# Optimization experiments

Hardware: AMD Instinct MI355X
Metric: run time of the kernel (lower is better)

The kernel has to match this reference:

```python
import jax, jax.numpy as jnp
import numpy as np

B, K, D = 16384, 2048, 128
T = 1.0

def setup_inputs() -> dict:
    key = jax.random.key(0)
    k1, k2 = jax.random.split(key)
    x = jax.random.normal(k1, (B, D), dtype=jnp.float32)
    # nn.init.normal_(center, std=0.01)
    center = jax.random.normal(k2, (K, D), dtype=jnp.float32) * 0.01
    return {"x": x, "center": center}

def _forward(x, center, temp):
    # Euclidean distance x[B,D] vs center[K,D] via expansion (avoids BxKxD blowup)
    x2 = jnp.sum(x * x, axis=-1, keepdims=True)          # [B,1]
    c2 = jnp.sum(center * center, axis=-1)               # [K]
    d2 = jnp.maximum(x2 + c2[None, :] - 2.0 * (x @ center.T), 0.0)  # [B,K]
    att_logit = -jnp.sqrt(d2) / temp                     # [B,K]
    # original detaches logits before softargmax
    logits = jax.lax.stop_gradient(att_logit)
    y_soft = jax.nn.softmax(logits / temp, axis=-1)      # [B,K]
    label = jnp.argmax(y_soft, axis=-1, keepdims=True)   # [B,1]
    y_hard = jax.nn.one_hot(label[:, 0], K, dtype=y_soft.dtype)  # [B,K]
    # straight-through estimator
    result = y_hard - jax.lax.stop_gradient(y_soft) + y_soft
    out = result @ center                                # [B,D]
    return out, center, label

def reference(x, center):
    return _forward(x, center, T)
```

## Files before the change

kernel.cpp:

```cpp
#include <hip/hip_runtime.h>
#include <cstdint>

#define NB 16384
#define NK 2048
#define ND 128
#define MARGIN 0.10f
#define CAP 2048
#define XPITCH 132

typedef __attribute__((ext_vector_type(8))) short bf16x8;
typedef __attribute__((ext_vector_type(4))) float f32x4;
typedef unsigned long long u64;

__device__ __forceinline__ unsigned short f2bf(float f) {
    unsigned u = __float_as_uint(f);
    u += 0x7fffu + ((u >> 16) & 1u);
    return (unsigned short)(u >> 16);
}

__global__ __launch_bounds__(256)
void prep(const float* __restrict__ c,
          unsigned short* __restrict__ cbf,
          float* __restrict__ c2,
          float* __restrict__ out_center) {
    const int bid = blockIdx.x;
    const int tid = threadIdx.x;
    if (bid < 128) {
        int t = bid * 256 + tid;
        int lane = t & 63, s = (t >> 6) & 3, kt = t >> 8;
        int kc = kt * 16 + (lane & 15);
        int d0 = s * 32 + (lane >> 4) * 8;
        const float* src = c + (long)kc * ND + d0;
        unsigned short h[8];
#pragma unroll
        for (int j = 0; j < 8; ++j) h[j] = f2bf(src[j]);
        int4 pk;
        pk.x = h[0] | (h[1] << 16); pk.y = h[2] | (h[3] << 16);
        pk.z = h[4] | (h[5] << 16); pk.w = h[6] | (h[7] << 16);
        ((int4*)cbf)[t] = pk;
    } else if (bid < 136) {
        int k = (bid - 128) * 256 + tid;
        const float4* row = (const float4*)(c + (long)k * ND);
        float s = 0.f;
#pragma unroll 8
        for (int i = 0; i < ND / 4; ++i) {
            float4 v = row[i];
            s += v.x * v.x + v.y * v.y + v.z * v.z + v.w * v.w;
        }
        c2[k] = s;
    } else {
        int i = (bid - 136) * 256 + tid;
        ((float4*)out_center)[i] = ((const float4*)c)[i];
    }
}

__global__ __launch_bounds__(512, 4)
void kmeans_main(const float* __restrict__ x,
                 const float* __restrict__ center,
                 const unsigned short* __restrict__ cbf,
                 const float* __restrict__ c2,
                 float* __restrict__ out,
                 float* __restrict__ label_out) {
    __shared__ float xs[32 * XPITCH];
    __shared__ float x2s[32];
    __shared__ unsigned bmin[32];
    __shared__ u64 best[32];
    __shared__ unsigned buf[CAP];
    __shared__ unsigned cnt;

    const int tid  = threadIdx.x;
    const int lane = tid & 63;
    const int wave = __builtin_amdgcn_readfirstlane(tid >> 6);
    const long rb  = (long)blockIdx.x * 32;

    {
        int idx = tid;
        int r = idx >> 5, q = idx & 31;
        ((float4*)(xs + r * XPITCH))[q] = ((const float4*)(x + (rb + r) * ND))[q];
        idx = tid + 512;
        r = idx >> 5; q = idx & 31;
        ((float4*)(xs + r * XPITCH))[q] = ((const float4*)(x + (rb + r) * ND))[q];
    }
    if (tid < 32) { bmin[tid] = 0x7f800000u; best[tid] = ~0ULL; }
    if (tid == 0) cnt = 0;
    __syncthreads();

    for (int i = 0; i < 4; ++i) {
        int r = wave * 4 + i;
        float2 v = *(const float2*)(xs + r * XPITCH + lane * 2);
        float s = v.x * v.x + v.y * v.y;
#pragma unroll
        for (int off = 32; off; off >>= 1) s += __shfl_xor(s, off, 64);
        if (lane == 0) x2s[r] = s;
    }
    __syncthreads();

    bf16x8 af[2][4];
#pragma unroll
    for (int rt = 0; rt < 2; ++rt)
#pragma unroll
        for (int s = 0; s < 4; ++s) {
            const float* p = xs + (rt * 16 + (lane & 15)) * XPITCH
                               + s * 32 + (lane >> 4) * 8;
            float4 u0 = ((const float4*)p)[0];
            float4 u1 = ((const float4*)p)[1];
            bf16x8 a;
            a[0] = (short)f2bf(u0.x); a[1] = (short)f2bf(u0.y);
            a[2] = (short)f2bf(u0.z); a[3] = (short)f2bf(u0.w);
            a[4] = (short)f2bf(u1.x); a[5] = (short)f2bf(u1.y);
            a[6] = (short)f2bf(u1.z); a[7] = (short)f2bf(u1.w);
            af[rt][s] = a;
        }

    float x2p[2][4];
#pragma unroll
    for (int rt = 0; rt < 2; ++rt)
#pragma unroll
        for (int reg = 0; reg < 4; ++reg)
            x2p[rt][reg] = x2s[rt * 16 + (lane >> 4) * 4 + reg];

    const bf16x8* CF = (const bf16x8*)cbf;
    const int kbase = wave * 256;

    float rmin[2][4];
#pragma unroll
    for (int rt = 0; rt < 2; ++rt)
#pragma unroll
        for (int reg = 0; reg < 4; ++reg) rmin[rt][reg] = __builtin_inff();

#pragma unroll 2
    for (int ct = 0; ct < 16; ++ct) {
        const int kt = (kbase >> 4) + ct;
        bf16x8 bf[4];
#pragma unroll
        for (int s = 0; s < 4; ++s) bf[s] = CF[(kt * 4 + s) * 64 + lane];
        f32x4 acc0 = {0.f,0.f,0.f,0.f}, acc1 = {0.f,0.f,0.f,0.f};
#pragma unroll
        for (int s = 0; s < 4; ++s) {
            acc0 = __builtin_amdgcn_mfma_f32_16x16x32_bf16(af[0][s], bf[s], acc0, 0,0,0);
            acc1 = __builtin_amdgcn_mfma_f32_16x16x32_bf16(af[1][s], bf[s], acc1, 0,0,0);
        }
        float c2v = c2[kt * 16 + (lane & 15)];
#pragma unroll
        for (int reg = 0; reg < 4; ++reg) {
            rmin[0][reg] = fminf(rmin[0][reg], fmaf(-2.f, acc0[reg], x2p[0][reg] + c2v));
            rmin[1][reg] = fminf(rmin[1][reg], fmaf(-2.f, acc1[reg], x2p[1][reg] + c2v));
        }
    }

#pragma unroll
    for (int rt = 0; rt < 2; ++rt)
#pragma unroll
        for (int reg = 0; reg < 4; ++reg) {
            float v = rmin[rt][reg];
#pragma unroll
            for (int off = 1; off < 16; off <<= 1)
                v = fminf(v, __shfl_xor(v, off, 64));
            if ((lane & 15) == 0)
                atomicMin(&bmin[rt * 16 + (lane >> 4) * 4 + reg], __float_as_uint(v));
        }
    __syncthreads();

    float thr[2][4];
#pragma unroll
    for (int rt = 0; rt < 2; ++rt)
#pragma unroll
        for (int reg = 0; reg < 4; ++reg)
            thr[rt][reg] = __uint_as_float(bmin[rt * 16 + (lane >> 4) * 4 + reg]) + MARGIN;

#pragma unroll 2
    for (int ct = 0; ct < 16; ++ct) {
        const int kt = (kbase >> 4) + ct;
        bf16x8 bf[4];
#pragma unroll
        for (int s = 0; s < 4; ++s) bf[s] = CF[(kt * 4 + s) * 64 + lane];
        f32x4 acc0 = {0.f,0.f,0.f,0.f}, acc1 = {0.f,0.f,0.f,0.f};
#pragma unroll
        for (int s = 0; s < 4; ++s) {
            acc0 = __builtin_amdgcn_mfma_f32_16x16x32_bf16(af[0][s], bf[s], acc0, 0,0,0);
            acc1 = __builtin_amdgcn_mfma_f32_16x16x32_bf16(af[1][s], bf[s], acc1, 0,0,0);
        }
        float c2v = c2[kt * 16 + (lane & 15)];
        const int col = kt * 16 + (lane & 15);
#pragma unroll
        for (int reg = 0; reg < 4; ++reg) {
            float d20 = fmaf(-2.f, acc0[reg], x2p[0][reg] + c2v);
            if (d20 <= thr[0][reg]) {
                unsigned rloc = (lane >> 4) * 4 + reg;
                unsigned idx = atomicAdd(&cnt, 1u);
                if (idx < CAP) buf[idx] = (rloc << 11) | (unsigned)col;
            }
            float d21 = fmaf(-2.f, acc1[reg], x2p[1][reg] + c2v);
            if (d21 <= thr[1][reg]) {
                unsigned rloc = 16 + (lane >> 4) * 4 + reg;
                unsigned idx = atomicAdd(&cnt, 1u);
                if (idx < CAP) buf[idx] = (rloc << 11) | (unsigned)col;
            }
        }
    }
    __syncthreads();

    unsigned n = cnt; if (n > CAP) n = CAP;
    for (unsigned i = tid; i < n; i += 512) {
        unsigned pc = buf[i];
        int rloc = pc >> 11, col = pc & (NK - 1);
        const float* xr = xs + rloc * XPITCH;
        const float* cr = center + (long)col * ND;
        float dot = 0.f;
#pragma unroll 8
        for (int d = 0; d < ND; ++d) dot = fmaf(xr[d], cr[d], dot);
        float t = x2s[rloc] + c2[col];
        float f = fmaxf(fmaf(-2.0f, dot, t), 0.0f);
        float s = __builtin_sqrtf(f);
        u64 key = ((u64)__float_as_uint(s) << 32) | (unsigned)col;
        atomicMin(&best[rloc], key);
    }
    __syncthreads();

    for (int i = 0; i < 4; ++i) {
        int rloc = wave * 4 + i;
        int bk = (int)(best[rloc] & 0xffffffffULL);
        float2 cv = ((const float2*)(center + (long)bk * ND))[lane];
        ((float2*)(out + (rb + rloc) * ND))[lane] = cv;
        if (lane == 0) label_out[rb + rloc] = (float)bk;
    }
}

extern "C" void kernel_launch(void* const* d_in, const int* in_sizes, int n_in,
                              void* d_out, int out_size, void* d_ws, size_t ws_size,
                              hipStream_t stream) {
    const float* x      = (const float*)d_in[0];
    const float* center = (const float*)d_in[1];
    float* out = (float*)d_out;

    float* out_x      = out;
    float* out_center = out + (long)NB * ND;
    float* out_label  = out_center + (long)NK * ND;

    unsigned short* cbf = (unsigned short*)d_ws;
    float* c2 = (float*)(cbf + (size_t)NK * ND);

    prep<<<392, 256, 0, stream>>>(center, cbf, c2, out_center);
    kmeans_main<<<NB / 32, 512, 0, stream>>>(x, center, cbf, c2,
                                             out_x, out_label);
}
```

Before: 97.67 us.

## Double rows per block to 64 and cache center norms in LDS

Each block now handles 64 query rows instead of 32. Every wave runs four 16-row MFMA tiles against each center fragment it loads, so each bf16 center load from global/L2 is reused twice as much. The center squared norms are staged once into shared memory rather than read from global inside the loops. In exchange, register and LDS use per block grow, occupancy drops to 2 blocks per CU, the grid halves to 256 blocks, and the candidate buffer of 2048 now serves twice as many rows, so it is more likely to overflow.

```diff
diff --git a/kernel.cpp b/kernel.cpp
--- a/kernel.cpp
+++ b/kernel.cpp
@@ -54,39 +54,38 @@
     }
 }
 
-__global__ __launch_bounds__(512, 4)
+__global__ __launch_bounds__(512, 2)
 void kmeans_main(const float* __restrict__ x,
                  const float* __restrict__ center,
                  const unsigned short* __restrict__ cbf,
                  const float* __restrict__ c2,
                  float* __restrict__ out,
                  float* __restrict__ label_out) {
-    __shared__ float xs[32 * XPITCH];
-    __shared__ float x2s[32];
-    __shared__ unsigned bmin[32];
-    __shared__ u64 best[32];
+    __shared__ float xs[64 * XPITCH];
+    __shared__ float c2s[NK];
+    __shared__ float x2s[64];
+    __shared__ unsigned bmin[64];
+    __shared__ u64 best[64];
     __shared__ unsigned buf[CAP];
     __shared__ unsigned cnt;
 
     const int tid  = threadIdx.x;
     const int lane = tid & 63;
     const int wave = __builtin_amdgcn_readfirstlane(tid >> 6);
-    const long rb  = (long)blockIdx.x * 32;
-
-    {
-        int idx = tid;
-        int r = idx >> 5, q = idx & 31;
+    const long rb  = (long)blockIdx.x * 64;
+
+#pragma unroll
+    for (int t = tid; t < 64 * 32; t += 512) {
+        int r = t >> 5, q = t & 31;
         ((float4*)(xs + r * XPITCH))[q] = ((const float4*)(x + (rb + r) * ND))[q];
-        idx = tid + 512;
-        r = idx >> 5; q = idx & 31;
-        ((float4*)(xs + r * XPITCH))[q] = ((const float4*)(x + (rb + r) * ND))[q];
-    }
-    if (tid < 32) { bmin[tid] = 0x7f800000u; best[tid] = ~0ULL; }
+    }
+    ((float4*)c2s)[tid] = ((const float4*)c2)[tid];
+    if (tid < 64) { bmin[tid] = 0x7f800000u; best[tid] = ~0ULL; }
     if (tid == 0) cnt = 0;
     __syncthreads();
 
-    for (int i = 0; i < 4; ++i) {
-        int r = wave * 4 + i;
+    for (int i = 0; i < 8; ++i) {
+        int r = wave * 8 + i;
         float2 v = *(const float2*)(xs + r * XPITCH + lane * 2);
         float s = v.x * v.x + v.y * v.y;
 #pragma unroll
@@ -95,9 +94,9 @@
     }
     __syncthreads();
 
-    bf16x8 af[2][4];
-#pragma unroll
-    for (int rt = 0; rt < 2; ++rt)
+    bf16x8 af[4][4];
+#pragma unroll
+    for (int rt = 0; rt < 4; ++rt)
 #pragma unroll
         for (int s = 0; s < 4; ++s) {
             const float* p = xs + (rt * 16 + (lane & 15)) * XPITCH
@@ -112,44 +111,47 @@
             af[rt][s] = a;
         }
 
-    float x2p[2][4];
-#pragma unroll
-    for (int rt = 0; rt < 2; ++rt)
+    float x2p[4][4];
+#pragma unroll
+    for (int rt = 0; rt < 4; ++rt)
 #pragma unroll
         for (int reg = 0; reg < 4; ++reg)
             x2p[rt][reg] = x2s[rt * 16 + (lane >> 4) * 4 + reg];
 
     const bf16x8* CF = (const bf16x8*)cbf;
-    const int kbase = wave * 256;
-
-    float rmin[2][4];
-#pragma unroll
-    for (int rt = 0; rt < 2; ++rt)
+    const int kt0 = (wave * 256) >> 4;
+
+    float rmin[4][4];
+#pragma unroll
+    for (int rt = 0; rt < 4; ++rt)
 #pragma unroll
         for (int reg = 0; reg < 4; ++reg) rmin[rt][reg] = __builtin_inff();
 
-#pragma unroll 2
+#pragma unroll 1
     for (int ct = 0; ct < 16; ++ct) {
-        const int kt = (kbase >> 4) + ct;
+        const int kt = kt0 + ct;
         bf16x8 bf[4];
 #pragma unroll
         for (int s = 0; s < 4; ++s) bf[s] = CF[(kt * 4 + s) * 64 + lane];
-        f32x4 acc0 = {0.f,0.f,0.f,0.f}, acc1 = {0.f,0.f,0.f,0.f};
-#pragma unroll
-        for (int s = 0; s < 4; ++s) {
-            acc0 = __builtin_amdgcn_mfma_f32_16x16x32_bf16(af[0][s], bf[s], acc0, 0,0,0);
-            acc1 = __builtin_amdgcn_mfma_f32_16x16x32_bf16(af[1][s], bf[s], acc1, 0,0,0);
-        }
-        float c2v = c2[kt * 16 + (lane & 15)];
-#pragma unroll
-        for (int reg = 0; reg < 4; ++reg) {
-            rmin[0][reg] = fminf(rmin[0][reg], fmaf(-2.f, acc0[reg], x2p[0][reg] + c2v));
-            rmin[1][reg] = fminf(rmin[1][reg], fmaf(-2.f, acc1[reg], x2p[1][reg] + c2v));
-        }
-    }
-
-#pragma unroll
-    for (int rt = 0; rt < 2; ++rt)
+        f32x4 acc[4];
+#pragma unroll
+        for (int rt = 0; rt < 4; ++rt) acc[rt] = (f32x4){0.f, 0.f, 0.f, 0.f};
+#pragma unroll
+        for (int s = 0; s < 4; ++s)
+#pragma unroll
+            for (int rt = 0; rt < 4; ++rt)
+                acc[rt] = __builtin_amdgcn_mfma_f32_16x16x32_bf16(af[rt][s], bf[s], acc[rt], 0,0,0);
+        float c2v = c2s[kt * 16 + (lane & 15)];
+#pragma unroll
+        for (int rt = 0; rt < 4; ++rt)
+#pragma unroll
+            for (int reg = 0; reg < 4; ++reg)
+                rmin[rt][reg] = fminf(rmin[rt][reg],
+                                      fmaf(-2.f, acc[rt][reg], x2p[rt][reg] + c2v));
+    }
+
+#pragma unroll
+    for (int rt = 0; rt < 4; ++rt)
 #pragma unroll
         for (int reg = 0; reg < 4; ++reg) {
             float v = rmin[rt][reg];
@@ -161,42 +163,40 @@
         }
     __syncthreads();
 
-    float thr[2][4];
-#pragma unroll
-    for (int rt = 0; rt < 2; ++rt)
+    float thr[4][4];
+#pragma unroll
+    for (int rt = 0; rt < 4; ++rt)
 #pragma unroll
         for (int reg = 0; reg < 4; ++reg)
             thr[rt][reg] = __uint_as_float(bmin[rt * 16 + (lane >> 4) * 4 + reg]) + MARGIN;
 
-#pragma unroll 2
+#pragma unroll 1
     for (int ct = 0; ct < 16; ++ct) {
-        const int kt = (kbase >> 4) + ct;
+        const int kt = kt0 + ct;
         bf16x8 bf[4];
 #pragma unroll
         for (int s = 0; s < 4; ++s) bf[s] = CF[(kt * 4 + s) * 64 + lane];
-        f32x4 acc0 = {0.f,0.f,0.f,0.f}, acc1 = {0.f,0.f,0.f,0.f};
-#pragma unroll
-        for (int s = 0; s < 4; ++s) {
-            acc0 = __builtin_amdgcn_mfma_f32_16x16x32_bf16(af[0][s], bf[s], acc0, 0,0,0);
-            acc1 = __builtin_amdgcn_mfma_f32_16x16x32_bf16(af[1][s], bf[s], acc1, 0,0,0);
-        }
-        float c2v = c2[kt * 16 + (lane & 15)];
+        f32x4 acc[4];
+#pragma unroll
+        for (int rt = 0; rt < 4; ++rt) acc[rt] = (f32x4){0.f, 0.f, 0.f, 0.f};
+#pragma unroll
+        for (int s = 0; s < 4; ++s)
+#pragma unroll
+            for (int rt = 0; rt < 4; ++rt)
+                acc[rt] = __builtin_amdgcn_mfma_f32_16x16x32_bf16(af[rt][s], bf[s], acc[rt], 0,0,0);
+        float c2v = c2s[kt * 16 + (lane & 15)];
         const int col = kt * 16 + (lane & 15);
 #pragma unroll
-        for (int reg = 0; reg < 4; ++reg) {
-            float d20 = fmaf(-2.f, acc0[reg], x2p[0][reg] + c2v);
-            if (d20 <= thr[0][reg]) {
-                unsigned rloc = (lane >> 4) * 4 + reg;
-                unsigned idx = atomicAdd(&cnt, 1u);
-                if (idx < CAP) buf[idx] = (rloc << 11) | (unsigned)col;
+        for (int rt = 0; rt < 4; ++rt)
+#pragma unroll
+            for (int reg = 0; reg < 4; ++reg) {
+                float d2a = fmaf(-2.f, acc[rt][reg], x2p[rt][reg] + c2v);
+                if (d2a <= thr[rt][reg]) {
+                    unsigned rloc = rt * 16 + (lane >> 4) * 4 + reg;
+                    unsigned idx = atomicAdd(&cnt, 1u);
+                    if (idx < CAP) buf[idx] = (rloc << 11) | (unsigned)col;
+                }
             }
-            float d21 = fmaf(-2.f, acc1[reg], x2p[1][reg] + c2v);
-            if (d21 <= thr[1][reg]) {
-                unsigned rloc = 16 + (lane >> 4) * 4 + reg;
-                unsigned idx = atomicAdd(&cnt, 1u);
-                if (idx < CAP) buf[idx] = (rloc << 11) | (unsigned)col;
-            }
-        }
     }
     __syncthreads();
 
@@ -209,7 +209,7 @@
         float dot = 0.f;
 #pragma unroll 8
         for (int d = 0; d < ND; ++d) dot = fmaf(xr[d], cr[d], dot);
-        float t = x2s[rloc] + c2[col];
+        float t = x2s[rloc] + c2s[col];
         float f = fmaxf(fmaf(-2.0f, dot, t), 0.0f);
         float s = __builtin_sqrtf(f);
         u64 key = ((u64)__float_as_uint(s) << 32) | (unsigned)col;
@@ -217,8 +217,8 @@
     }
     __syncthreads();
 
-    for (int i = 0; i < 4; ++i) {
-        int rloc = wave * 4 + i;
+    for (int i = 0; i < 8; ++i) {
+        int rloc = wave * 8 + i;
         int bk = (int)(best[rloc] & 0xffffffffULL);
         float2 cv = ((const float2*)(center + (long)bk * ND))[lane];
         ((float2*)(out + (rb + rloc) * ND))[lane] = cv;
@@ -241,6 +241,6 @@
     float* c2 = (float*)(cbf + (size_t)NK * ND);
 
     prep<<<392, 256, 0, stream>>>(center, cbf, c2, out_center);
-    kmeans_main<<<NB / 32, 512, 0, stream>>>(x, center, cbf, c2,
+    kmeans_main<<<NB / 64, 512, 0, stream>>>(x, center, cbf, c2,
                                              out_x, out_label);
 }
```

Result: slower. 103.7 us (+6.2%).

## Merge two-pass distance scan into single pass with running per-wave threshold

Applied to the files above, without the earlier changes.

Replaces the two MFMA passes (block-wide min, then candidate collection) with one pass. Each wave keeps a running row minimum via 16-lane shuffle reductions and collects candidates within the margin of that local running min, which drops the second GEMM and a block barrier. Candidate counts can grow because the running threshold is looser early and per-wave rather than block-wide, so CAP is raised to 6144. c2 is also staged in LDS. The extra LDS, the per-tile shuffles and the larger refinement workload may lower occupancy and add cost.

```diff
diff --git a/kernel.cpp b/kernel.cpp
--- a/kernel.cpp
+++ b/kernel.cpp
@@ -5,7 +5,7 @@
 #define NK 2048
 #define ND 128
 #define MARGIN 0.10f
-#define CAP 2048
+#define CAP 6144
 #define XPITCH 132
 
 typedef __attribute__((ext_vector_type(8))) short bf16x8;
@@ -62,8 +62,8 @@
                  float* __restrict__ out,
                  float* __restrict__ label_out) {
     __shared__ float xs[32 * XPITCH];
+    __shared__ float c2s[NK];
     __shared__ float x2s[32];
-    __shared__ unsigned bmin[32];
     __shared__ u64 best[32];
     __shared__ unsigned buf[CAP];
     __shared__ unsigned cnt;
@@ -81,7 +81,8 @@
         r = idx >> 5; q = idx & 31;
         ((float4*)(xs + r * XPITCH))[q] = ((const float4*)(x + (rb + r) * ND))[q];
     }
-    if (tid < 32) { bmin[tid] = 0x7f800000u; best[tid] = ~0ULL; }
+    ((float4*)c2s)[tid] = ((const float4*)c2)[tid];
+    if (tid < 32) best[tid] = ~0ULL;
     if (tid == 0) cnt = 0;
     __syncthreads();
 
@@ -120,17 +121,17 @@
             x2p[rt][reg] = x2s[rt * 16 + (lane >> 4) * 4 + reg];
 
     const bf16x8* CF = (const bf16x8*)cbf;
-    const int kbase = wave * 256;
-
-    float rmin[2][4];
+    const int kt0 = wave * 16;
+
+    float rowmin[2][4];
 #pragma unroll
     for (int rt = 0; rt < 2; ++rt)
 #pragma unroll
-        for (int reg = 0; reg < 4; ++reg) rmin[rt][reg] = __builtin_inff();
-
-#pragma unroll 2
+        for (int reg = 0; reg < 4; ++reg) rowmin[rt][reg] = __builtin_inff();
+
+#pragma unroll 1
     for (int ct = 0; ct < 16; ++ct) {
-        const int kt = (kbase >> 4) + ct;
+        const int kt = kt0 + ct;
         bf16x8 bf[4];
 #pragma unroll
         for (int s = 0; s < 4; ++s) bf[s] = CF[(kt * 4 + s) * 64 + lane];
@@ -140,58 +141,26 @@
             acc0 = __builtin_amdgcn_mfma_f32_16x16x32_bf16(af[0][s], bf[s], acc0, 0,0,0);
             acc1 = __builtin_amdgcn_mfma_f32_16x16x32_bf16(af[1][s], bf[s], acc1, 0,0,0);
         }
-        float c2v = c2[kt * 16 + (lane & 15)];
-#pragma unroll
-        for (int reg = 0; reg < 4; ++reg) {
-            rmin[0][reg] = fminf(rmin[0][reg], fmaf(-2.f, acc0[reg], x2p[0][reg] + c2v));
-            rmin[1][reg] = fminf(rmin[1][reg], fmaf(-2.f, acc1[reg], x2p[1][reg] + c2v));
-        }
-    }
-
-#pragma unroll
-    for (int rt = 0; rt < 2; ++rt)
-#pragma unroll
-        for (int reg = 0; reg < 4; ++reg) {
-            float v = rmin[rt][reg];
-#pragma unroll
-            for (int off = 1; off < 16; off <<= 1)
-                v = fminf(v, __shfl_xor(v, off, 64));
-            if ((lane & 15) == 0)
-                atomicMin(&bmin[rt * 16 + (lane >> 4) * 4 + reg], __float_as_uint(v));
-        }
-    __syncthreads();
-
-    float thr[2][4];
-#pragma unroll
-    for (int rt = 0; rt < 2; ++rt)
-#pragma unroll
-        for (int reg = 0; reg < 4; ++reg)
-            thr[rt][reg] = __uint_as_float(bmin[rt * 16 + (lane >> 4) * 4 + reg]) + MARGIN;
-
-#pragma unroll 2
-    for (int ct = 0; ct < 16; ++ct) {
-        const int kt = (kbase >> 4) + ct;
-        bf16x8 bf[4];
-#pragma unroll
-        for (int s = 0; s < 4; ++s) bf[s] = CF[(kt * 4 + s) * 64 + lane];
-        f32x4 acc0 = {0.f,0.f,0.f,0.f}, acc1 = {0.f,0.f,0.f,0.f};
-#pragma unroll
-        for (int s = 0; s < 4; ++s) {
-            acc0 = __builtin_amdgcn_mfma_f32_16x16x32_bf16(af[0][s], bf[s], acc0, 0,0,0);
-            acc1 = __builtin_amdgcn_mfma_f32_16x16x32_bf16(af[1][s], bf[s], acc1, 0,0,0);
-        }
-        float c2v = c2[kt * 16 + (lane & 15)];
+        float c2v = c2s[kt * 16 + (lane & 15)];
         const int col = kt * 16 + (lane & 15);
 #pragma unroll
         for (int reg = 0; reg < 4; ++reg) {
             float d20 = fmaf(-2.f, acc0[reg], x2p[0][reg] + c2v);
-            if (d20 <= thr[0][reg]) {
+            float d21 = fmaf(-2.f, acc1[reg], x2p[1][reg] + c2v);
+            float m0 = d20, m1 = d21;
+#pragma unroll
+            for (int off = 1; off < 16; off <<= 1) {
+                m0 = fminf(m0, __shfl_xor(m0, off, 64));
+                m1 = fminf(m1, __shfl_xor(m1, off, 64));
+            }
+            rowmin[0][reg] = fminf(rowmin[0][reg], m0);
+            rowmin[1][reg] = fminf(rowmin[1][reg], m1);
+            if (d20 <= rowmin[0][reg] + MARGIN) {
                 unsigned rloc = (lane >> 4) * 4 + reg;
                 unsigned idx = atomicAdd(&cnt, 1u);
                 if (idx < CAP) buf[idx] = (rloc << 11) | (unsigned)col;
             }
-            float d21 = fmaf(-2.f, acc1[reg], x2p[1][reg] + c2v);
-            if (d21 <= thr[1][reg]) {
+            if (d21 <= rowmin[1][reg] + MARGIN) {
                 unsigned rloc = 16 + (lane >> 4) * 4 + reg;
                 unsigned idx = atomicAdd(&cnt, 1u);
                 if (idx < CAP) buf[idx] = (rloc << 11) | (unsigned)col;
@@ -209,7 +178,7 @@
         float dot = 0.f;
 #pragma unroll 8
         for (int d = 0; d < ND; ++d) dot = fmaf(xr[d], cr[d], dot);
-        float t = x2s[rloc] + c2[col];
+        float t = x2s[rloc] + c2s[col];
         float f = fmaxf(fmaf(-2.0f, dot, t), 0.0f);
         float s = __builtin_sqrtf(f);
         u64 key = ((u64)__float_as_uint(s) << 32) | (unsigned)col;
```

After: 164.5 us. 1.68x slower.

## Fuse two-pass distance filter into one pass with fp16-cached distances

Applied to the files above, without the earlier changes.

The second full MFMA pass over all centers is replaced by caching each tile's partial distance (d2 - x2, stored as fp16 pairs) in registers. The 2048 centers are processed in four chunks, with a block-level running minimum and threshold filter after each chunk, so the MFMA GEMM runs only once. Squared center norms move into shared memory, candidate entries become 16-bit, and the buffer capacity and margin grow. The cost is extra barriers per chunk, looser early thresholds that admit more candidates for exact fp32 rescoring, more registers and more LDS.

```diff
diff --git a/kernel.cpp b/kernel.cpp
--- a/kernel.cpp
+++ b/kernel.cpp
@@ -4,8 +4,8 @@
 #define NB 16384
 #define NK 2048
 #define ND 128
-#define MARGIN 0.10f
-#define CAP 2048
+#define MARGINF 0.11f
+#define CAP 6144
 #define XPITCH 132
 
 typedef __attribute__((ext_vector_type(8))) short bf16x8;
@@ -17,6 +17,8 @@
     u += 0x7fffu + ((u >> 16) & 1u);
     return (unsigned short)(u >> 16);
 }
+
+union HU { _Float16 h; unsigned short s; };
 
 __global__ __launch_bounds__(256)
 void prep(const float* __restrict__ c,
@@ -62,10 +64,11 @@
                  float* __restrict__ out,
                  float* __restrict__ label_out) {
     __shared__ float xs[32 * XPITCH];
+    __shared__ float c2s[NK];
     __shared__ float x2s[32];
     __shared__ unsigned bmin[32];
     __shared__ u64 best[32];
-    __shared__ unsigned buf[CAP];
+    __shared__ unsigned short buf[CAP];
     __shared__ unsigned cnt;
 
     const int tid  = threadIdx.x;
@@ -81,6 +84,7 @@
         r = idx >> 5; q = idx & 31;
         ((float4*)(xs + r * XPITCH))[q] = ((const float4*)(x + (rb + r) * ND))[q];
     }
+    ((float4*)c2s)[tid] = ((const float4*)c2)[tid];
     if (tid < 32) { bmin[tid] = 0x7f800000u; best[tid] = ~0ULL; }
     if (tid == 0) cnt = 0;
     __syncthreads();
@@ -120,7 +124,7 @@
             x2p[rt][reg] = x2s[rt * 16 + (lane >> 4) * 4 + reg];
 
     const bf16x8* CF = (const bf16x8*)cbf;
-    const int kbase = wave * 256;
+    const int kt0 = wave * 16;
 
     float rmin[2][4];
 #pragma unroll
@@ -128,73 +132,74 @@
 #pragma unroll
         for (int reg = 0; reg < 4; ++reg) rmin[rt][reg] = __builtin_inff();
 
-#pragma unroll 2
-    for (int ct = 0; ct < 16; ++ct) {
-        const int kt = (kbase >> 4) + ct;
-        bf16x8 bf[4];
-#pragma unroll
-        for (int s = 0; s < 4; ++s) bf[s] = CF[(kt * 4 + s) * 64 + lane];
-        f32x4 acc0 = {0.f,0.f,0.f,0.f}, acc1 = {0.f,0.f,0.f,0.f};
-#pragma unroll
-        for (int s = 0; s < 4; ++s) {
-            acc0 = __builtin_amdgcn_mfma_f32_16x16x32_bf16(af[0][s], bf[s], acc0, 0,0,0);
-            acc1 = __builtin_amdgcn_mfma_f32_16x16x32_bf16(af[1][s], bf[s], acc1, 0,0,0);
-        }
-        float c2v = c2[kt * 16 + (lane & 15)];
-#pragma unroll
-        for (int reg = 0; reg < 4; ++reg) {
-            rmin[0][reg] = fminf(rmin[0][reg], fmaf(-2.f, acc0[reg], x2p[0][reg] + c2v));
-            rmin[1][reg] = fminf(rmin[1][reg], fmaf(-2.f, acc1[reg], x2p[1][reg] + c2v));
-        }
-    }
-
-#pragma unroll
-    for (int rt = 0; rt < 2; ++rt)
-#pragma unroll
-        for (int reg = 0; reg < 4; ++reg) {
-            float v = rmin[rt][reg];
-#pragma unroll
-            for (int off = 1; off < 16; off <<= 1)
-                v = fminf(v, __shfl_xor(v, off, 64));
-            if ((lane & 15) == 0)
-                atomicMin(&bmin[rt * 16 + (lane >> 4) * 4 + reg], __float_as_uint(v));
-        }
-    __syncthreads();
-
-    float thr[2][4];
-#pragma unroll
-    for (int rt = 0; rt < 2; ++rt)
-#pragma unroll
-        for (int reg = 0; reg < 4; ++reg)
-            thr[rt][reg] = __uint_as_float(bmin[rt * 16 + (lane >> 4) * 4 + reg]) + MARGIN;
-
-#pragma unroll 2
-    for (int ct = 0; ct < 16; ++ct) {
-        const int kt = (kbase >> 4) + ct;
-        bf16x8 bf[4];
-#pragma unroll
-        for (int s = 0; s < 4; ++s) bf[s] = CF[(kt * 4 + s) * 64 + lane];
-        f32x4 acc0 = {0.f,0.f,0.f,0.f}, acc1 = {0.f,0.f,0.f,0.f};
-#pragma unroll
-        for (int s = 0; s < 4; ++s) {
-            acc0 = __builtin_amdgcn_mfma_f32_16x16x32_bf16(af[0][s], bf[s], acc0, 0,0,0);
-            acc1 = __builtin_amdgcn_mfma_f32_16x16x32_bf16(af[1][s], bf[s], acc1, 0,0,0);
-        }
-        float c2v = c2[kt * 16 + (lane & 15)];
-        const int col = kt * 16 + (lane & 15);
-#pragma unroll
-        for (int reg = 0; reg < 4; ++reg) {
-            float d20 = fmaf(-2.f, acc0[reg], x2p[0][reg] + c2v);
-            if (d20 <= thr[0][reg]) {
-                unsigned rloc = (lane >> 4) * 4 + reg;
-                unsigned idx = atomicAdd(&cnt, 1u);
-                if (idx < CAP) buf[idx] = (rloc << 11) | (unsigned)col;
-            }
-            float d21 = fmaf(-2.f, acc1[reg], x2p[1][reg] + c2v);
-            if (d21 <= thr[1][reg]) {
-                unsigned rloc = 16 + (lane >> 4) * 4 + reg;
-                unsigned idx = atomicAdd(&cnt, 1u);
-                if (idx < CAP) buf[idx] = (rloc << 11) | (unsigned)col;
+    for (int chunk = 0; chunk < 4; ++chunk) {
+        unsigned rc[4][4];
+
+#pragma unroll
+        for (int ct = 0; ct < 4; ++ct) {
+            const int kt = kt0 + chunk * 4 + ct;
+            bf16x8 bfr[4];
+#pragma unroll
+            for (int s = 0; s < 4; ++s) bfr[s] = CF[(kt * 4 + s) * 64 + lane];
+            f32x4 acc0 = {0.f,0.f,0.f,0.f}, acc1 = {0.f,0.f,0.f,0.f};
+#pragma unroll
+            for (int s = 0; s < 4; ++s) {
+                acc0 = __builtin_amdgcn_mfma_f32_16x16x32_bf16(af[0][s], bfr[s], acc0, 0,0,0);
+                acc1 = __builtin_amdgcn_mfma_f32_16x16x32_bf16(af[1][s], bfr[s], acc1, 0,0,0);
+            }
+            float c2v = c2s[kt * 16 + (lane & 15)];
+#pragma unroll
+            for (int reg = 0; reg < 4; ++reg) {
+                float d20 = fmaf(-2.f, acc0[reg], x2p[0][reg] + c2v);
+                float d21 = fmaf(-2.f, acc1[reg], x2p[1][reg] + c2v);
+                rmin[0][reg] = fminf(rmin[0][reg], d20);
+                rmin[1][reg] = fminf(rmin[1][reg], d21);
+                HU a; a.h = (_Float16)(d20 - x2p[0][reg]);
+                HU b; b.h = (_Float16)(d21 - x2p[1][reg]);
+                rc[ct][reg] = (unsigned)a.s | ((unsigned)b.s << 16);
+            }
+        }
+
+#pragma unroll
+        for (int rt = 0; rt < 2; ++rt)
+#pragma unroll
+            for (int reg = 0; reg < 4; ++reg) {
+                float v = rmin[rt][reg];
+#pragma unroll
+                for (int off = 1; off < 16; off <<= 1)
+                    v = fminf(v, __shfl_xor(v, off, 64));
+                if ((lane & 15) == 0)
+                    atomicMin(&bmin[rt * 16 + (lane >> 4) * 4 + reg], __float_as_uint(v));
+            }
+        __syncthreads();
+
+        float rthr[2][4];
+#pragma unroll
+        for (int rt = 0; rt < 2; ++rt)
+#pragma unroll
+            for (int reg = 0; reg < 4; ++reg)
+                rthr[rt][reg] = __uint_as_float(bmin[rt * 16 + (lane >> 4) * 4 + reg])
+                                + MARGINF - x2p[rt][reg];
+
+#pragma unroll
+        for (int ct = 0; ct < 4; ++ct) {
+            const int col = (kt0 + chunk * 4 + ct) * 16 + (lane & 15);
+#pragma unroll
+            for (int reg = 0; reg < 4; ++reg) {
+                unsigned v = rc[ct][reg];
+                HU a; a.s = (unsigned short)(v & 0xffffu);
+                HU b; b.s = (unsigned short)(v >> 16);
+                float lo = (float)a.h, hi = (float)b.h;
+                if (lo <= rthr[0][reg]) {
+                    unsigned rloc = (lane >> 4) * 4 + reg;
+                    unsigned idx = atomicAdd(&cnt, 1u);
+                    if (idx < CAP) buf[idx] = (unsigned short)((rloc << 11) | col);
+                }
+                if (hi <= rthr[1][reg]) {
+                    unsigned rloc = 16 + (lane >> 4) * 4 + reg;
+                    unsigned idx = atomicAdd(&cnt, 1u);
+                    if (idx < CAP) buf[idx] = (unsigned short)((rloc << 11) | col);
+                }
             }
         }
     }
@@ -209,7 +214,7 @@
         float dot = 0.f;
 #pragma unroll 8
         for (int d = 0; d < ND; ++d) dot = fmaf(xr[d], cr[d], dot);
-        float t = x2s[rloc] + c2[col];
+        float t = x2s[rloc] + c2s[col];
         float f = fmaxf(fmaf(-2.0f, dot, t), 0.0f);
         float s = __builtin_sqrtf(f);
         u64 key = ((u64)__float_as_uint(s) << 32) | (unsigned)col;
```

After: 101.2 us. +3.6%, slower.
